# Performance work log

Hardware: AMD Instinct MI355X
Metric: run time of the kernel (lower is better)

The kernel has to match this reference:

```python
import jax, jax.numpy as jnp
import numpy as np

COMMITMENT_COST = 0.25


def setup_inputs() -> dict:
    key = jax.random.key(0)
    k1, k2 = jax.random.split(key)
    N, K, D = 65536, 8192, 64
    z_e = jax.random.normal(k1, (N, D), dtype=jnp.float32)
    # xavier_uniform for Embedding(K, D): limit = sqrt(6/(K+D))
    limit = float(np.sqrt(6.0 / (K + D)))
    codebook = jax.random.uniform(k2, (K, D), dtype=jnp.float32, minval=-limit, maxval=limit)
    return {"z_e": z_e, "codebook": codebook}


def reference(z_e, codebook):
    # Squared Euclidean distances; argmin over d^2 == argmin over cdist(p=2)
    x2 = jnp.sum(z_e * z_e, axis=-1, keepdims=True)            # [N,1]
    e2 = jnp.sum(codebook * codebook, axis=-1)                 # [K]
    d2 = x2 - 2.0 * (z_e @ codebook.T) + e2                    # [N,K]
    encoding_indices = jnp.argmin(d2, axis=-1)                 # [N] int

    z_q = codebook[encoding_indices]                           # [N,D] gather

    sg = jax.lax.stop_gradient
    codebook_loss = jnp.mean((z_q - sg(z_e)) ** 2)
    commitment_loss = jnp.mean((z_e - sg(z_q)) ** 2)
    vq_loss = codebook_loss + COMMITMENT_COST * commitment_loss

    # straight-through estimator
    z_q_st = z_e + sg(z_q - z_e)
    return z_q_st, vq_loss, encoding_indices
```

## Files before the change

### kernel.cpp

```cpp
#include <hip/hip_runtime.h>
#include <hip/hip_bf16.h>

#define N_PTS 65536
#define K_CB  8192
#define D_DIM 64
#define CAPS  63

typedef float f32x4 __attribute__((ext_vector_type(4)));
typedef short s16x8 __attribute__((ext_vector_type(8)));

typedef __attribute__((address_space(1))) const unsigned int gu32;
typedef __attribute__((address_space(3))) unsigned int lu32;

__device__ __forceinline__ unsigned bfpack2(float a, float b) {
    union { __hip_bfloat162 h2; unsigned u; } cv;
    cv.h2 = __float22bfloat162_rn(make_float2(a, b));
    return cv.u;
}

__device__ __forceinline__ void gl2lds16(const void* g, void* lds) {
    __builtin_amdgcn_global_load_lds((gu32*)g, (lu32*)lds, 16, 0, 0);
}

template <int CTRL>
__device__ __forceinline__ float dpp_fmax(float v) {
    int s = __builtin_amdgcn_update_dpp(0, __float_as_int(v), CTRL, 0xf, 0xf, true);
    return fmaxf(v, __int_as_float(s));
}

__global__ __launch_bounds__(256) void vq_pack(
        const float* __restrict__ cb, unsigned short* __restrict__ cbswz) {
    int g = blockIdx.x * 256 + threadIdx.x;
    int row = g >> 3, s = g & 7;
    int u = (s ^ (row & 7)) * 8;
    const float4* p = (const float4*)(cb + (size_t)row * D_DIM + u);
    float4 a = p[0], b = p[1];
    uint4 pk;
    pk.x = bfpack2(a.x, a.y); pk.y = bfpack2(a.z, a.w);
    pk.z = bfpack2(b.x, b.y); pk.w = bfpack2(b.z, b.w);
    *(uint4*)(cbswz + (size_t)row * 64 + s * 8) = pk;
}

__global__ __launch_bounds__(256) void vq_prep(
        const float* __restrict__ z, const float* __restrict__ cb,
        float* __restrict__ e2, float* __restrict__ x2, float* __restrict__ bmax) {
#pragma clang fp contract(off)
    __shared__ float sm[4];
    int b = blockIdx.x;
    int lane = threadIdx.x & 63;
    int wv = threadIdx.x >> 6;
    const float* src; float* dst; int row0;
    if (b < 128) { src = cb; dst = e2; row0 = b * 64 + wv * 16; }
    else         { src = z;  dst = x2; row0 = (b - 128) * 64 + wv * 16; }
    float lmax = 0.f;
    for (int r = 0; r < 16; ++r) {
        int row = row0 + r;
        float v = src[(size_t)row * D_DIM + lane];
        float w = v * v;
        float ra = w;
#pragma unroll
        for (int i = 1; i < 8; ++i) ra = ra + __shfl(w, lane + 8 * i, 64);
        float r0 = __shfl(ra, 0, 64), r1 = __shfl(ra, 1, 64),
              r2 = __shfl(ra, 2, 64), r3 = __shfl(ra, 3, 64),
              r4 = __shfl(ra, 4, 64), r5 = __shfl(ra, 5, 64),
              r6 = __shfl(ra, 6, 64), r7 = __shfl(ra, 7, 64);
        if (lane == 0) {
            float s = ((r0 + r1) + (r2 + r3)) + ((r4 + r5) + (r6 + r7));
            dst[row] = s;
            lmax = fmaxf(lmax, s);
        }
    }
    if (b < 128) {
        if (lane == 0) sm[wv] = lmax;
        __syncthreads();
        if (threadIdx.x == 0)
            bmax[b] = fmaxf(fmaxf(sm[0], sm[1]), fmaxf(sm[2], sm[3]));
    }
}

__device__ __forceinline__ void stage_chunk(
        const unsigned short* __restrict__ cbswz, const float* __restrict__ e2,
        unsigned short* bufb, float* e2hb, int kc, int w, int l) {
    const char* gbase = (const char*)(cbswz + (size_t)kc * 256 * 64);
#pragma unroll
    for (int j = 0; j < 8; ++j) {
        int off = j * 4096 + w * 1024;
        gl2lds16(gbase + off + l * 16, (char*)bufb + off);
    }
    if (w == 0)
        gl2lds16(e2 + kc * 256 + l * 4, e2hb);
}

__global__ __launch_bounds__(256, 2) void vq_coarse(
        const float* __restrict__ z, const unsigned short* __restrict__ cbswz,
        const float* __restrict__ e2, const float* __restrict__ x2,
        const float* __restrict__ bmax, int* __restrict__ cand) {
    __shared__ __align__(16) unsigned short pool[4][128 * 64];
    __shared__ __align__(16) float e2h[2][256];
    __shared__ int cntS[128];
    const int tid = threadIdx.x;
    const int w = tid >> 6, l = tid & 63, tx = l & 15, q = l >> 4;
    const int n0 = blockIdx.x * 128;

    if (tid < 128) cntS[tid] = 0;

#pragma unroll
    for (int i = 0; i < 4; ++i) {
        int lin = tid + 256 * i;
        int row = lin >> 3, u = lin & 7;
        const float4* p = (const float4*)(z + (size_t)(n0 + row) * D_DIM + u * 8);
        float4 a = p[0], b2 = p[1];
        uint4 pk;
        pk.x = bfpack2(a.x, a.y);   pk.y = bfpack2(a.z, a.w);
        pk.z = bfpack2(b2.x, b2.y); pk.w = bfpack2(b2.z, b2.w);
        *(uint4*)&pool[0][row * 64 + ((u ^ (row & 7)) * 8)] = pk;
    }

    float e2m;
    {
        float v = fmaxf(bmax[l], bmax[l + 64]);
#pragma unroll
        for (int m = 1; m < 64; m <<= 1) v = fmaxf(v, __shfl_xor(v, m, 64));
        e2m = v;
    }

    float halfW[8], A[8], M[8];
#pragma unroll
    for (int i = 0; i < 8; ++i) {
        int row = n0 + w * 32 + (i >> 2) * 16 + q * 4 + (i & 3);
        halfW[i] = 0.0175f * sqrtf(x2[row] * e2m) + 1e-4f;
        A[i] = 3.0e38f;
        M[i] = -3.4e38f;
    }

    __syncthreads();
    s16x8 afr[2][2];
#pragma unroll
    for (int rt = 0; rt < 2; ++rt)
#pragma unroll
        for (int ks = 0; ks < 2; ++ks) {
            int row = w * 32 + rt * 16 + tx;
            afr[rt][ks] = *(const s16x8*)&pool[0][row * 64 + (((ks * 4 + q) ^ (tx & 7)) * 8)];
        }
    __syncthreads();

    stage_chunk(cbswz, e2, &pool[0][0], e2h[0], 0, w, l);
    __syncthreads();

    for (int it = 0; it < 33; ++it) {
        const int kc = (it < 32) ? it : 0;
        const int cur = it & 1;
        if (it < 32)
            stage_chunk(cbswz, e2, &pool[((it + 1) & 1) * 2][0], e2h[(it + 1) & 1],
                        (it + 1 < 32) ? it + 1 : 0, w, l);

        const unsigned short* cbb = &pool[cur * 2][0];
        const float* e2c = e2h[cur];
        const bool collect = (it > 0);
        for (int ct = 0; ct < 16; ++ct) {
            int crow = ct * 16 + tx;
            float bias = -0.5f * e2c[crow];
            s16x8 b0 = *(const s16x8*)&cbb[crow * 64 + ((q ^ (tx & 7)) * 8)];
            s16x8 b1 = *(const s16x8*)&cbb[crow * 64 + (((4 + q) ^ (tx & 7)) * 8)];
            int kglob = kc * 256 + crow;
#pragma unroll
            for (int rt = 0; rt < 2; ++rt) {
                f32x4 acc = {bias, bias, bias, bias};
                acc = __builtin_amdgcn_mfma_f32_16x16x32_bf16(afr[rt][0], b0, acc, 0, 0, 0);
                acc = __builtin_amdgcn_mfma_f32_16x16x32_bf16(afr[rt][1], b1, acc, 0, 0, 0);
                const int i0 = rt * 4;
                M[i0 + 0] = fmaxf(M[i0 + 0], acc[0]);
                M[i0 + 1] = fmaxf(M[i0 + 1], acc[1]);
                M[i0 + 2] = fmaxf(M[i0 + 2], acc[2]);
                M[i0 + 3] = fmaxf(M[i0 + 3], acc[3]);
                bool any = (acc[0] >= A[i0 + 0]) | (acc[1] >= A[i0 + 1]) |
                           (acc[2] >= A[i0 + 2]) | (acc[3] >= A[i0 + 3]);
                if (collect && any) {
#pragma unroll
                    for (int r = 0; r < 4; ++r) {
                        if (acc[r] >= A[i0 + r]) {
                            int row = w * 32 + rt * 16 + q * 4 + r;
                            int slot = atomicAdd(&cntS[row], 1);
                            if (slot < CAPS)
                                cand[(size_t)(n0 + row) * 64 + slot] = kglob;
                        }
                    }
                }
            }
        }
        if (it < 32) {
#pragma unroll
            for (int i = 0; i < 8; ++i) {
                float v = M[i];
                v = dpp_fmax<0xB1>(v);
                v = dpp_fmax<0x4E>(v);
                v = dpp_fmax<0x124>(v);
                v = dpp_fmax<0x128>(v);
                M[i] = v;
                A[i] = v - halfW[i];
            }
        }
        __syncthreads();
    }
    if (tid < 128) cand[(size_t)(n0 + tid) * 64 + 63] = cntS[tid];
}

__device__ __forceinline__ float exact_score(const float* zr, const float* __restrict__ cb,
                                             const float* __restrict__ e2, float x2v, int k) {
    const float4* c4 = (const float4*)(cb + (size_t)k * D_DIM);
    float g = 0.f;
#pragma unroll
    for (int j = 0; j < 16; ++j) {
        float4 v = c4[j];
        g = fmaf(zr[4 * j + 0], v.x, g);
        g = fmaf(zr[4 * j + 1], v.y, g);
        g = fmaf(zr[4 * j + 2], v.z, g);
        g = fmaf(zr[4 * j + 3], v.w, g);
    }
    return fmaf(-2.f, g, x2v) + e2[k];
}

__global__ __launch_bounds__(256, 2) void vq_rescore(
        const float* __restrict__ z, const float* __restrict__ cb,
        const float* __restrict__ e2, const float* __restrict__ x2,
        int* __restrict__ slots, float* __restrict__ idx_out,
        float* __restrict__ partials) {
    int tid = threadIdx.x;
    int n = blockIdx.x * 256 + tid;
    float zr[64];
    const float4* z4 = (const float4*)(z + (size_t)n * D_DIM);
#pragma unroll
    for (int i = 0; i < 16; ++i) {
        float4 v = z4[i];
        zr[4 * i] = v.x; zr[4 * i + 1] = v.y; zr[4 * i + 2] = v.z; zr[4 * i + 3] = v.w;
    }
    float x2v = x2[n];
    int cnt = slots[(size_t)n * 64 + 63];
    float bs = 3.4e38f; int bk = 0x7fffffff;
    if (cnt <= CAPS) {
        int i = 0;
        for (; i + 1 < cnt; i += 2) {
            int ka = slots[(size_t)n * 64 + i];
            int kb = slots[(size_t)n * 64 + i + 1];
            float sa = exact_score(zr, cb, e2, x2v, ka);
            float sb = exact_score(zr, cb, e2, x2v, kb);
            if (sa < bs || (sa == bs && ka < bk)) { bs = sa; bk = ka; }
            if (sb < bs || (sb == bs && kb < bk)) { bs = sb; bk = kb; }
        }
        if (i < cnt) {
            int k = slots[(size_t)n * 64 + i];
            float s = exact_score(zr, cb, e2, x2v, k);
            if (s < bs || (s == bs && k < bk)) { bs = s; bk = k; }
        }
    }
    unsigned long long mask = __ballot(cnt > CAPS);
    while (mask) {
        int src = __ffsll((long long)mask) - 1;
        mask &= (mask - 1);
        int rown = __shfl(n, src, 64);
        float x2s = __shfl(x2v, src, 64);
        float zs[64];
        const float4* zz = (const float4*)(z + (size_t)rown * D_DIM);
#pragma unroll
        for (int i = 0; i < 16; ++i) {
            float4 v = zz[i];
            zs[4 * i] = v.x; zs[4 * i + 1] = v.y; zs[4 * i + 2] = v.z; zs[4 * i + 3] = v.w;
        }
        float fb = 3.4e38f; int fk = 0x7fffffff;
        for (int k = (tid & 63); k < K_CB; k += 64) {
            float s = exact_score(zs, cb, e2, x2s, k);
            if (s < fb || (s == fb && k < fk)) { fb = s; fk = k; }
        }
#pragma unroll
        for (int m = 1; m < 64; m <<= 1) {
            float ov = __shfl_xor(fb, m, 64);
            int   ok = __shfl_xor(fk, m, 64);
            if (ov < fb || (ov == fb && ok < fk)) { fb = ov; fk = ok; }
        }
        if ((tid & 63) == src) { bs = fb; bk = fk; }
    }
    idx_out[n] = (float)bk;
    __threadfence_block();

    float lsum = 0.f;
    const float4* c4 = (const float4*)(cb + (size_t)bk * D_DIM);
    float4* o4 = (float4*)((float*)slots + (size_t)n * 64);
#pragma unroll
    for (int j = 0; j < 16; ++j) {
        float4 c = c4[j];
        float4 o;
        float d0 = c.x - zr[4 * j];     o.x = zr[4 * j]     + d0;
        float d1 = c.y - zr[4 * j + 1]; o.y = zr[4 * j + 1] + d1;
        float d2 = c.z - zr[4 * j + 2]; o.z = zr[4 * j + 2] + d2;
        float d3 = c.w - zr[4 * j + 3]; o.w = zr[4 * j + 3] + d3;
        lsum += d0 * d0 + d1 * d1 + d2 * d2 + d3 * d3;
        o4[j] = o;
    }
    __shared__ float red[256];
    red[tid] = lsum;
    __syncthreads();
    for (int s = 128; s > 0; s >>= 1) {
        if (tid < s) red[tid] += red[tid + s];
        __syncthreads();
    }
    if (tid == 0) partials[blockIdx.x] = red[0];
}

__global__ void vq_final(const float* __restrict__ partials, float* __restrict__ loss_out) {
    __shared__ float red[256];
    int tid = threadIdx.x;
    red[tid] = partials[tid];
    __syncthreads();
    for (int s = 128; s > 0; s >>= 1) {
        if (tid < s) red[tid] += red[tid + s];
        __syncthreads();
    }
    if (tid == 0) *loss_out = 1.25f * red[0] / (float)(N_PTS * D_DIM);
}

extern "C" void kernel_launch(void* const* d_in, const int* in_sizes, int n_in,
                              void* d_out, int out_size, void* d_ws, size_t ws_size,
                              hipStream_t stream) {
    const float* z  = (const float*)d_in[0];
    const float* cb = (const float*)d_in[1];
    float* out      = (float*)d_out;
    float* zq_out   = out;
    float* loss_out = out + (size_t)N_PTS * D_DIM;
    float* idx_out  = loss_out + 1;

    float* wsf = (float*)d_ws;
    float* partials = wsf;
    float* e2 = wsf + 256;
    float* x2 = wsf + 256 + K_CB;
    unsigned short* cbswz = (unsigned short*)(wsf + 256 + K_CB + N_PTS);

    int* cand = (int*)zq_out;
    float* bmax = idx_out;

    vq_pack   <<<K_CB * 8 / 256, 256, 0, stream>>>(cb, cbswz);
    vq_prep   <<<128 + N_PTS / 64, 256, 0, stream>>>(z, cb, e2, x2, bmax);
    vq_coarse <<<N_PTS / 128, 256, 0, stream>>>(z, cbswz, e2, x2, bmax, cand);
    vq_rescore<<<N_PTS / 256, 256, 0, stream>>>(z, cb, e2, x2, cand, idx_out, partials);
    vq_final  <<<1, 256, 0, stream>>>(partials, loss_out);
}
```

Baseline: 339.2 us.

## Split coarse VQ block across 8 waves with 16 rows each and scalar threshold gate

Doubles the vq_coarse block to 512 threads so each wave handles one 16-row MFMA tile instead of two. Staging and z-load loops are re-split across the 8 waves. The per-element candidate test is gated by a single per-lane minimum threshold (Amin) in place of the collect flag, and the inner loop is unrolled by 4. This is meant to raise wave-level parallelism and cut VALU compare work, at the cost of loading each codebook B fragment from LDS once per 16 rows instead of once per 32.

Measured after the change: 275.9 us. 1.23x faster.

```diff
diff --git a/kernel.cpp b/kernel.cpp
--- a/kernel.cpp
+++ b/kernel.cpp
@@ -83,15 +83,15 @@
         unsigned short* bufb, float* e2hb, int kc, int w, int l) {
     const char* gbase = (const char*)(cbswz + (size_t)kc * 256 * 64);
 #pragma unroll
-    for (int j = 0; j < 8; ++j) {
-        int off = j * 4096 + w * 1024;
+    for (int j = 0; j < 4; ++j) {
+        int off = j * 8192 + w * 1024;
         gl2lds16(gbase + off + l * 16, (char*)bufb + off);
     }
     if (w == 0)
         gl2lds16(e2 + kc * 256 + l * 4, e2hb);
 }
 
-__global__ __launch_bounds__(256, 2) void vq_coarse(
+__global__ __launch_bounds__(512, 4) void vq_coarse(
         const float* __restrict__ z, const unsigned short* __restrict__ cbswz,
         const float* __restrict__ e2, const float* __restrict__ x2,
         const float* __restrict__ bmax, int* __restrict__ cand) {
@@ -105,8 +105,8 @@
     if (tid < 128) cntS[tid] = 0;
 
 #pragma unroll
-    for (int i = 0; i < 4; ++i) {
-        int lin = tid + 256 * i;
+    for (int i = 0; i < 2; ++i) {
+        int lin = tid + 512 * i;
         int row = lin >> 3, u = lin & 7;
         const float4* p = (const float4*)(z + (size_t)(n0 + row) * D_DIM + u * 8);
         float4 a = p[0], b2 = p[1];
@@ -124,24 +124,23 @@
         e2m = v;
     }
 
-    float halfW[8], A[8], M[8];
-#pragma unroll
-    for (int i = 0; i < 8; ++i) {
-        int row = n0 + w * 32 + (i >> 2) * 16 + q * 4 + (i & 3);
+    float halfW[4], A[4], M[4];
+#pragma unroll
+    for (int i = 0; i < 4; ++i) {
+        int row = n0 + w * 16 + q * 4 + i;
         halfW[i] = 0.0175f * sqrtf(x2[row] * e2m) + 1e-4f;
         A[i] = 3.0e38f;
         M[i] = -3.4e38f;
     }
-
-    __syncthreads();
-    s16x8 afr[2][2];
-#pragma unroll
-    for (int rt = 0; rt < 2; ++rt)
-#pragma unroll
-        for (int ks = 0; ks < 2; ++ks) {
-            int row = w * 32 + rt * 16 + tx;
-            afr[rt][ks] = *(const s16x8*)&pool[0][row * 64 + (((ks * 4 + q) ^ (tx & 7)) * 8)];
-        }
+    float Amin = 3.0e38f;
+
+    __syncthreads();
+    s16x8 afr[2];
+#pragma unroll
+    for (int ks = 0; ks < 2; ++ks) {
+        int row = w * 16 + tx;
+        afr[ks] = *(const s16x8*)&pool[0][row * 64 + (((ks * 4 + q) ^ (tx & 7)) * 8)];
+    }
     __syncthreads();
 
     stage_chunk(cbswz, e2, &pool[0][0], e2h[0], 0, w, l);
@@ -156,41 +155,36 @@
 
         const unsigned short* cbb = &pool[cur * 2][0];
         const float* e2c = e2h[cur];
-        const bool collect = (it > 0);
+#pragma unroll 4
         for (int ct = 0; ct < 16; ++ct) {
             int crow = ct * 16 + tx;
             float bias = -0.5f * e2c[crow];
             s16x8 b0 = *(const s16x8*)&cbb[crow * 64 + ((q ^ (tx & 7)) * 8)];
             s16x8 b1 = *(const s16x8*)&cbb[crow * 64 + (((4 + q) ^ (tx & 7)) * 8)];
-            int kglob = kc * 256 + crow;
-#pragma unroll
-            for (int rt = 0; rt < 2; ++rt) {
-                f32x4 acc = {bias, bias, bias, bias};
-                acc = __builtin_amdgcn_mfma_f32_16x16x32_bf16(afr[rt][0], b0, acc, 0, 0, 0);
-                acc = __builtin_amdgcn_mfma_f32_16x16x32_bf16(afr[rt][1], b1, acc, 0, 0, 0);
-                const int i0 = rt * 4;
-                M[i0 + 0] = fmaxf(M[i0 + 0], acc[0]);
-                M[i0 + 1] = fmaxf(M[i0 + 1], acc[1]);
-                M[i0 + 2] = fmaxf(M[i0 + 2], acc[2]);
-                M[i0 + 3] = fmaxf(M[i0 + 3], acc[3]);
-                bool any = (acc[0] >= A[i0 + 0]) | (acc[1] >= A[i0 + 1]) |
-                           (acc[2] >= A[i0 + 2]) | (acc[3] >= A[i0 + 3]);
-                if (collect && any) {
-#pragma unroll
-                    for (int r = 0; r < 4; ++r) {
-                        if (acc[r] >= A[i0 + r]) {
-                            int row = w * 32 + rt * 16 + q * 4 + r;
-                            int slot = atomicAdd(&cntS[row], 1);
-                            if (slot < CAPS)
-                                cand[(size_t)(n0 + row) * 64 + slot] = kglob;
-                        }
+            f32x4 acc = {bias, bias, bias, bias};
+            acc = __builtin_amdgcn_mfma_f32_16x16x32_bf16(afr[0], b0, acc, 0, 0, 0);
+            acc = __builtin_amdgcn_mfma_f32_16x16x32_bf16(afr[1], b1, acc, 0, 0, 0);
+            M[0] = fmaxf(M[0], acc[0]);
+            M[1] = fmaxf(M[1], acc[1]);
+            M[2] = fmaxf(M[2], acc[2]);
+            M[3] = fmaxf(M[3], acc[3]);
+            float amax = fmaxf(fmaxf(acc[0], acc[1]), fmaxf(acc[2], acc[3]));
+            if (amax >= Amin) {
+                int kglob = kc * 256 + crow;
+#pragma unroll
+                for (int r = 0; r < 4; ++r) {
+                    if (acc[r] >= A[r]) {
+                        int row = w * 16 + q * 4 + r;
+                        int slot = atomicAdd(&cntS[row], 1);
+                        if (slot < CAPS)
+                            cand[(size_t)(n0 + row) * 64 + slot] = kglob;
                     }
                 }
             }
         }
         if (it < 32) {
 #pragma unroll
-            for (int i = 0; i < 8; ++i) {
+            for (int i = 0; i < 4; ++i) {
                 float v = M[i];
                 v = dpp_fmax<0xB1>(v);
                 v = dpp_fmax<0x4E>(v);
@@ -199,6 +193,7 @@
                 M[i] = v;
                 A[i] = v - halfW[i];
             }
+            Amin = fminf(fminf(A[0], A[1]), fminf(A[2], A[3]));
         }
         __syncthreads();
     }
@@ -339,7 +334,7 @@
 
     vq_pack   <<<K_CB * 8 / 256, 256, 0, stream>>>(cb, cbswz);
     vq_prep   <<<128 + N_PTS / 64, 256, 0, stream>>>(z, cb, e2, x2, bmax);
-    vq_coarse <<<N_PTS / 128, 256, 0, stream>>>(z, cbswz, e2, x2, bmax, cand);
+    vq_coarse <<<N_PTS / 128, 512, 0, stream>>>(z, cbswz, e2, x2, bmax, cand);
     vq_rescore<<<N_PTS / 256, 256, 0, stream>>>(z, cb, e2, x2, cand, idx_out, partials);
     vq_final  <<<1, 256, 0, stream>>>(partials, loss_out);
 }
```
